# Optimization experiments

Hardware: AMD Instinct MI355X
Metric: run time of the kernel (lower is better)

## Reference

```python
import jax, jax.numpy as jnp
import numpy as np

N_NODES = 100000
N_EDGES = 1600000
NODE_DIM = 128
HIDDEN_DIM = 128


def _sage_conv(x, src, dst, deg_inv, W_l, W_r, b):
    # PyG SAGEConv (aggr='mean', root_weight=True):
    #   out = lin_l(mean_{j in N(i)} x_j) + lin_r(x_i)
    msgs = x[src]                                             # [E, d_in] gather
    agg = jax.ops.segment_sum(msgs, dst, num_segments=N_NODES)  # [N, d_in]
    mean = agg * deg_inv[:, None]
    return mean @ W_l + x @ W_r + b


def setup_inputs() -> dict:
    key = jax.random.key(0)
    ks = jax.random.split(key, 9)
    x = jax.random.normal(ks[0], (N_NODES, NODE_DIM), dtype=jnp.float32)
    edge_index = jax.random.randint(ks[1], (2, N_EDGES), 0, N_NODES, dtype=jnp.int32)
    t = jnp.zeros((1,), dtype=jnp.float32)

    def glorot(k, fan_in, fan_out):
        s = (6.0 / (fan_in + fan_out)) ** 0.5
        return jax.random.uniform(k, (fan_in, fan_out), jnp.float32, -s, s)

    return {
        "t": t,
        "x": x,
        "edge_index": edge_index,
        "W1_l": glorot(ks[2], NODE_DIM, HIDDEN_DIM),
        "W1_r": glorot(ks[3], NODE_DIM, HIDDEN_DIM),
        "b1": jnp.zeros((HIDDEN_DIM,), jnp.float32),
        "W2_l": glorot(ks[4], HIDDEN_DIM, HIDDEN_DIM),
        "W2_r": glorot(ks[5], HIDDEN_DIM, HIDDEN_DIM),
        "b2": jnp.zeros((HIDDEN_DIM,), jnp.float32),
        "W3_l": glorot(ks[6], HIDDEN_DIM, NODE_DIM),
        "W3_r": glorot(ks[7], HIDDEN_DIM, NODE_DIM),
        "b3": jnp.zeros((NODE_DIM,), jnp.float32),
    }


def reference(t, x, edge_index, W1_l, W1_r, b1, W2_l, W2_r, b2, W3_l, W3_r, b3):
    src, dst = edge_index[0], edge_index[1]
    deg = jax.ops.segment_sum(jnp.ones((N_EDGES,), x.dtype), dst, num_segments=N_NODES)
    deg_inv = jnp.where(deg > 0, 1.0 / jnp.maximum(deg, 1.0), 0.0)

    h = jax.nn.relu(_sage_conv(x, src, dst, deg_inv, W1_l, W1_r, b1))
    h = jax.nn.relu(_sage_conv(h, src, dst, deg_inv, W2_l, W2_r, b2))
    dx_dt = _sage_conv(h, src, dst, deg_inv, W3_l, W3_r, b3)
    return dx_dt
```

## Files before the change

kernel.cpp:

```cpp
#include <hip/hip_runtime.h>

#define NN   100000
#define NE   1600000
#define DIM  128
#define NBKT 391
#define EPB  16384
#define NBLK 98
#define NTILES (NN / 16)
#define CASTB 12500
#define CWB   384

typedef short          s16x8 __attribute__((ext_vector_type(8)));
typedef unsigned short u16x8 __attribute__((ext_vector_type(8)));
typedef float          f32x4 __attribute__((ext_vector_type(4)));

__device__ __forceinline__ unsigned short f2b(float f) {
    unsigned u = __float_as_uint(f);
    unsigned r = ((u >> 16) & 1u) + 0x7FFFu;
    return (unsigned short)((u + r) >> 16);
}
__device__ __forceinline__ float b2f(unsigned short h) {
    return __uint_as_float(((unsigned)h) << 16);
}

__global__ void k_prep(const float* __restrict__ x, unsigned short* __restrict__ xb,
                       const int* __restrict__ dst, int* __restrict__ hist,
                       const float* __restrict__ W1l, const float* __restrict__ W1r,
                       const float* __restrict__ W2l, const float* __restrict__ W2r,
                       const float* __restrict__ W3l, const float* __restrict__ W3r,
                       unsigned short* __restrict__ Wt1, unsigned short* __restrict__ Wt2,
                       unsigned short* __restrict__ Wt3) {
    __shared__ int lh[NBKT];
    int t = threadIdx.x, b = blockIdx.x;
    if (b < NBLK) {
        for (int j = t; j < NBKT; j += 256) lh[j] = 0;
        __syncthreads();
        int base = b * EPB;
        int end = base + EPB; if (end > NE) end = NE;
        for (int i = base + t; i < end; i += 256) atomicAdd(&lh[dst[i] >> 8], 1);
        __syncthreads();
        for (int j = t; j < NBKT; j += 256) hist[j * NBLK + b] = lh[j];
    } else if (b < NBLK + CASTB) {
        int i = (b - NBLK) * 256 + t;
        float4 v = ((const float4*)x)[i];
        ushort4 o;
        o.x = f2b(v.x); o.y = f2b(v.y); o.z = f2b(v.z); o.w = f2b(v.w);
        ((ushort4*)xb)[i] = o;
    } else {
        int i = (b - NBLK - CASTB) * 256 + t;
        int L = i >> 15;
        int rem = i & 32767;
        int n = rem >> 8;
        int k = rem & 255;
        const float* Wl = (L == 0) ? W1l : (L == 1) ? W2l : W3l;
        const float* Wr = (L == 0) ? W1r : (L == 1) ? W2r : W3r;
        unsigned short* Wt = (L == 0) ? Wt1 : (L == 1) ? Wt2 : Wt3;
        float v = (k < 128) ? Wl[k * 128 + n] : Wr[(k - 128) * 128 + n];
        Wt[n * 256 + k] = f2b(v);
    }
}

__global__ void k_scanrow(int* __restrict__ hist, int* __restrict__ row_total) {
    __shared__ int sh[128];
    int k = blockIdx.x, t = threadIdx.x;
    int v = (t < NBLK) ? hist[k * NBLK + t] : 0;
    sh[t] = v;
    __syncthreads();
    for (int off = 1; off < 128; off <<= 1) {
        int a = (t >= off) ? sh[t - off] : 0;
        __syncthreads();
        sh[t] += a;
        __syncthreads();
    }
    if (t < NBLK) hist[k * NBLK + t] = sh[t] - v;
    if (t == 127) row_total[k] = sh[127];
}

__global__ void k_scanbkt(const int* __restrict__ row_total, int* __restrict__ bbase) {
    __shared__ int sh[512];
    int t = threadIdx.x;
    int v = (t < NBKT) ? row_total[t] : 0;
    sh[t] = v;
    __syncthreads();
    for (int off = 1; off < 512; off <<= 1) {
        int a = (t >= off) ? sh[t - off] : 0;
        __syncthreads();
        sh[t] += a;
        __syncthreads();
    }
    if (t < NBKT) bbase[t] = sh[t] - v;
    if (t == NBKT) bbase[NBKT] = NE;
}

__global__ void k_bin2(const int* __restrict__ src, const int* __restrict__ dst,
                       const int* __restrict__ hist, const int* __restrict__ bbase,
                       int* __restrict__ binned) {
    __shared__ int s_base[NBKT];
    __shared__ int s_cnt[NBKT];
    int t = threadIdx.x, b = blockIdx.x;
    for (int j = t; j < NBKT; j += 256) {
        s_base[j] = bbase[j] + hist[j * NBLK + b];
        s_cnt[j] = 0;
    }
    __syncthreads();
    int base = b * EPB;
    int end = base + EPB; if (end > NE) end = NE;
    for (int i = base + t; i < end; i += 256) {
        int d = dst[i];
        int k = d >> 8;
        int w = (src[i] << 8) | (d & 255);
        int lpos = atomicAdd(&s_cnt[k], 1);
        binned[s_base[k] + lpos] = w;
    }
}

__global__ void k_build(const int* __restrict__ binned,
                        const int* __restrict__ bucket_base,
                        int* __restrict__ csr,
                        int* __restrict__ row_start, int* __restrict__ deg,
                        float* __restrict__ deg_inv) {
    __shared__ int s_deg[256], s_scan[256], s_cur[256];
    __shared__ int stage[8192];
    int b = blockIdx.x, t = threadIdx.x;
    int base = bucket_base[b], end = bucket_base[b + 1];
    int cnt = end - base;
    s_deg[t] = 0;
    __syncthreads();
    for (int i = t; i < cnt; i += 256)
        atomicAdd(&s_deg[binned[base + i] & 255], 1);
    __syncthreads();
    s_scan[t] = s_deg[t];
    __syncthreads();
    for (int off = 1; off < 256; off <<= 1) {
        int a = (t >= off) ? s_scan[t - off] : 0;
        __syncthreads();
        s_scan[t] += a;
        __syncthreads();
    }
    int excl = s_scan[t] - s_deg[t];
    s_cur[t] = excl;
    int node = b * 256 + t;
    if (node < NN) {
        int d = s_deg[t];
        row_start[node] = base + excl;
        deg[node]       = d;
        deg_inv[node]   = (d > 0) ? 1.0f / (float)d : 0.0f;
    }
    __syncthreads();
    for (int i = t; i < cnt; i += 256) {
        int w = binned[base + i];
        int pos = atomicAdd(&s_cur[w & 255], 1);
        int s = w >> 8;
        if (pos < 8192) stage[pos] = s;
        else            csr[base + pos] = s;
    }
    __syncthreads();
    int m = cnt < 8192 ? cnt : 8192;
    for (int i = t; i < m; i += 256) csr[base + i] = stage[i];
}

__global__ void k_gather(const unsigned short* __restrict__ feat,
                         const int* __restrict__ row_start, const int* __restrict__ deg,
                         const float* __restrict__ deg_inv, const int* __restrict__ csr,
                         unsigned short* __restrict__ mean) {
    int lane = threadIdx.x & 63;
    int wv   = threadIdx.x >> 6;
    int n    = blockIdx.x * 4 + wv;
    int q = lane >> 4, c = lane & 15;
    int base = row_start[n];
    int d    = deg[n];
    float acc0[8], acc1[8];
#pragma unroll
    for (int t = 0; t < 8; t++) { acc0[t] = 0.0f; acc1[t] = 0.0f; }
    const u16x8* fp = (const u16x8*)feat;
    int j = q;
    for (; j + 4 < d; j += 8) {
        int s0 = csr[base + j];
        int s1 = csr[base + j + 4];
        u16x8 v0 = fp[s0 * 16 + c];
        u16x8 v1 = fp[s1 * 16 + c];
#pragma unroll
        for (int t = 0; t < 8; t++) { acc0[t] += b2f(v0[t]); acc1[t] += b2f(v1[t]); }
    }
    if (j < d) {
        int s0 = csr[base + j];
        u16x8 v0 = fp[s0 * 16 + c];
#pragma unroll
        for (int t = 0; t < 8; t++) acc0[t] += b2f(v0[t]);
    }
#pragma unroll
    for (int t = 0; t < 8; t++) acc0[t] += acc1[t];
#pragma unroll
    for (int t = 0; t < 8; t++) {
        acc0[t] += __shfl_xor(acc0[t], 16, 64);
        acc0[t] += __shfl_xor(acc0[t], 32, 64);
    }
    if (q == 0) {
        float s = deg_inv[n];
        u16x8 o;
#pragma unroll
        for (int t = 0; t < 8; t++) o[t] = f2b(acc0[t] * s);
        ((u16x8*)mean)[n * 16 + c] = o;
    }
}

template <int MODE>
__global__ void __launch_bounds__(512)
k_lin(const unsigned short* __restrict__ meanb,
      const unsigned short* __restrict__ hb,
      const unsigned short* __restrict__ Wt,
      const float* __restrict__ bias, void* __restrict__ out) {
    __shared__ s16x8 sW[4096];
    int t = threadIdx.x;
    const s16x8* wp = (const s16x8*)Wt;
#pragma unroll
    for (int it = 0; it < 8; it++) {
        int ci = it * 512 + t;
        int frag = ci >> 6, ln = ci & 63;
        int mt = frag >> 3, kt = frag & 7;
        int m = mt * 16 + (ln & 15);
        int kc = kt * 4 + (ln >> 4);
        sW[ci] = wp[m * 32 + kc];
    }
    __syncthreads();

    int lane = t & 63;
    int wv   = t >> 6;
    int tile = blockIdx.x * 8 + wv;
    if (tile >= NTILES) return;
    int n0 = tile * 16;
    int q = lane >> 4, c = lane & 15;
    const s16x8* mp = (const s16x8*)meanb;
    const s16x8* hp = (const s16x8*)hb;
    int row = n0 + c;
    s16x8 B[8];
#pragma unroll
    for (int kt = 0; kt < 4; kt++) B[kt] = mp[row * 16 + kt * 4 + q];
#pragma unroll
    for (int kt = 0; kt < 4; kt++) B[4 + kt] = hp[row * 16 + kt * 4 + q];
    const f32x4* bp = (const f32x4*)bias;
#pragma unroll
    for (int mt = 0; mt < 8; mt++) {
        f32x4 acc = {0.f, 0.f, 0.f, 0.f};
#pragma unroll
        for (int kt = 0; kt < 8; kt++)
            acc = __builtin_amdgcn_mfma_f32_16x16x32_bf16(sW[(mt * 8 + kt) * 64 + lane],
                                                          B[kt], acc, 0, 0, 0);
        f32x4 bv = bp[mt * 4 + q];
        int node = n0 + c;
        if (MODE == 0) {
            ushort4 o;
            float v0 = acc[0] + bv[0]; if (v0 < 0.f) v0 = 0.f;
            float v1 = acc[1] + bv[1]; if (v1 < 0.f) v1 = 0.f;
            float v2 = acc[2] + bv[2]; if (v2 < 0.f) v2 = 0.f;
            float v3 = acc[3] + bv[3]; if (v3 < 0.f) v3 = 0.f;
            o.x = f2b(v0); o.y = f2b(v1); o.z = f2b(v2); o.w = f2b(v3);
            ((ushort4*)out)[node * 32 + mt * 4 + q] = o;
        } else {
            f32x4 v;
#pragma unroll
            for (int r = 0; r < 4; r++) v[r] = acc[r] + bv[r];
            ((f32x4*)out)[node * 32 + mt * 4 + q] = v;
        }
    }
}

extern "C" void kernel_launch(void* const* d_in, const int* in_sizes, int n_in,
                              void* d_out, int out_size, void* d_ws, size_t ws_size,
                              hipStream_t stream) {
    const float* x   = (const float*)d_in[1];
    const int*   ei  = (const int*)d_in[2];
    const int*   src = ei;
    const int*   dst = ei + NE;
    const float* W1l = (const float*)d_in[3];
    const float* W1r = (const float*)d_in[4];
    const float* b1  = (const float*)d_in[5];
    const float* W2l = (const float*)d_in[6];
    const float* W2r = (const float*)d_in[7];
    const float* b2  = (const float*)d_in[8];
    const float* W3l = (const float*)d_in[9];
    const float* W3r = (const float*)d_in[10];
    const float* b3  = (const float*)d_in[11];

    char* w = (char*)d_ws;
    auto carve = [&](size_t bytes) {
        void* p = (void*)w;
        w += (bytes + 255) & ~(size_t)255;
        return p;
    };
    int*   row_start = (int*)carve(NN * 4);
    int*   deg       = (int*)carve(NN * 4);
    float* deg_inv   = (float*)carve(NN * 4);
    int*   hist      = (int*)carve((size_t)NBKT * NBLK * 4);
    int*   row_total = (int*)carve(NBKT * 4);
    int*   bbase     = (int*)carve((NBKT + 1) * 4);
    int*   csr       = (int*)carve((size_t)NE * 4);
    unsigned short* Wt1 = (unsigned short*)carve(128 * 256 * 2);
    unsigned short* Wt2 = (unsigned short*)carve(128 * 256 * 2);
    unsigned short* Wt3 = (unsigned short*)carve(128 * 256 * 2);
    unsigned short* xb    = (unsigned short*)carve((size_t)NN * DIM * 2);
    unsigned short* meanb = (unsigned short*)carve((size_t)NN * DIM * 2);
    unsigned short* h1b   = (unsigned short*)carve((size_t)NN * DIM * 2);
    unsigned short* h2b   = xb;
    int*   binned    = (int*)meanb;

    k_prep<<<NBLK + CASTB + CWB, 256, 0, stream>>>(x, xb, dst, hist,
                                                   W1l, W1r, W2l, W2r, W3l, W3r,
                                                   Wt1, Wt2, Wt3);
    k_scanrow<<<NBKT, 128, 0, stream>>>(hist, row_total);
    k_scanbkt<<<1, 512, 0, stream>>>(row_total, bbase);
    k_bin2<<<NBLK, 256, 0, stream>>>(src, dst, hist, bbase, binned);
    k_build<<<NBKT, 256, 0, stream>>>(binned, bbase, csr, row_start, deg, deg_inv);

    const int GB = NN / 4;
    const int LB = (NTILES + 7) / 8;

    k_gather<<<GB, 256, 0, stream>>>(xb, row_start, deg, deg_inv, csr, meanb);
    k_lin<0><<<LB, 512, 0, stream>>>(meanb, xb, Wt1, b1, (void*)h1b);
    k_gather<<<GB, 256, 0, stream>>>(h1b, row_start, deg, deg_inv, csr, meanb);
    k_lin<0><<<LB, 512, 0, stream>>>(meanb, h1b, Wt2, b2, (void*)h2b);
    k_gather<<<GB, 256, 0, stream>>>(h2b, row_start, deg, deg_inv, csr, meanb);
    k_lin<1><<<LB, 512, 0, stream>>>(meanb, h2b, Wt3, b3, d_out);
}
```

Measured before the change: 451.6 us.

## Fuse CSR preprocessing kernels into one cooperative kernel with grid syncs

Replaces the five preprocessing launches (histogram/cast, row scan, bucket scan, binning, CSR build) with a single cooperative kernel of 512 blocks that separates the phases with grid-wide syncs. Edges are repartitioned across 512 blocks instead of 98, so the histogram and binning phases use more of the GPU, and the row scan now handles 512 entries per bucket. This removes per-launch overhead and idle gaps between the small kernels. In exchange, each grid sync has a cost, the cast loops become grid-stride, and correctness depends on all 512 blocks being co-resident.

```diff
diff --git a/kernel.cpp b/kernel.cpp
--- a/kernel.cpp
+++ b/kernel.cpp
@@ -1,14 +1,17 @@
 #include <hip/hip_runtime.h>
+#include <hip/hip_cooperative_groups.h>
+
+namespace cg = cooperative_groups;
 
 #define NN   100000
 #define NE   1600000
 #define DIM  128
 #define NBKT 391
-#define EPB  16384
-#define NBLK 98
+#define GRID 512
+#define EPB3 (NE / GRID)
+#define NX4  (NN * DIM / 4)
+#define NWELE (3 * 128 * 256)
 #define NTILES (NN / 16)
-#define CASTB 12500
-#define CWB   384
 
 typedef short          s16x8 __attribute__((ext_vector_type(8)));
 typedef unsigned short u16x8 __attribute__((ext_vector_type(8)));
@@ -23,140 +26,140 @@
     return __uint_as_float(((unsigned)h) << 16);
 }
 
-__global__ void k_prep(const float* __restrict__ x, unsigned short* __restrict__ xb,
-                       const int* __restrict__ dst, int* __restrict__ hist,
-                       const float* __restrict__ W1l, const float* __restrict__ W1r,
-                       const float* __restrict__ W2l, const float* __restrict__ W2r,
-                       const float* __restrict__ W3l, const float* __restrict__ W3r,
-                       unsigned short* __restrict__ Wt1, unsigned short* __restrict__ Wt2,
-                       unsigned short* __restrict__ Wt3) {
-    __shared__ int lh[NBKT];
+__global__ void __launch_bounds__(256)
+k_prep_all(const float* __restrict__ x, unsigned short* __restrict__ xb,
+           const int* __restrict__ src, const int* __restrict__ dst,
+           int* __restrict__ hist, int* __restrict__ row_total,
+           int* __restrict__ bbase, int* __restrict__ binned, int* __restrict__ csr,
+           int* __restrict__ row_start, int* __restrict__ deg,
+           float* __restrict__ deg_inv,
+           const float* __restrict__ W1l, const float* __restrict__ W1r,
+           const float* __restrict__ W2l, const float* __restrict__ W2r,
+           const float* __restrict__ W3l, const float* __restrict__ W3r,
+           unsigned short* __restrict__ Wt1, unsigned short* __restrict__ Wt2,
+           unsigned short* __restrict__ Wt3) {
+    __shared__ int shm[8960];
+    cg::grid_group grid = cg::this_grid();
     int t = threadIdx.x, b = blockIdx.x;
-    if (b < NBLK) {
+    int e0 = b * EPB3, e1 = e0 + EPB3;
+
+    {
+        int* lh = shm;
         for (int j = t; j < NBKT; j += 256) lh[j] = 0;
         __syncthreads();
-        int base = b * EPB;
-        int end = base + EPB; if (end > NE) end = NE;
-        for (int i = base + t; i < end; i += 256) atomicAdd(&lh[dst[i] >> 8], 1);
-        __syncthreads();
-        for (int j = t; j < NBKT; j += 256) hist[j * NBLK + b] = lh[j];
-    } else if (b < NBLK + CASTB) {
-        int i = (b - NBLK) * 256 + t;
-        float4 v = ((const float4*)x)[i];
-        ushort4 o;
-        o.x = f2b(v.x); o.y = f2b(v.y); o.z = f2b(v.z); o.w = f2b(v.w);
-        ((ushort4*)xb)[i] = o;
-    } else {
-        int i = (b - NBLK - CASTB) * 256 + t;
-        int L = i >> 15;
-        int rem = i & 32767;
-        int n = rem >> 8;
-        int k = rem & 255;
-        const float* Wl = (L == 0) ? W1l : (L == 1) ? W2l : W3l;
-        const float* Wr = (L == 0) ? W1r : (L == 1) ? W2r : W3r;
-        unsigned short* Wt = (L == 0) ? Wt1 : (L == 1) ? Wt2 : Wt3;
-        float v = (k < 128) ? Wl[k * 128 + n] : Wr[(k - 128) * 128 + n];
-        Wt[n * 256 + k] = f2b(v);
-    }
-}
-
-__global__ void k_scanrow(int* __restrict__ hist, int* __restrict__ row_total) {
-    __shared__ int sh[128];
-    int k = blockIdx.x, t = threadIdx.x;
-    int v = (t < NBLK) ? hist[k * NBLK + t] : 0;
-    sh[t] = v;
-    __syncthreads();
-    for (int off = 1; off < 128; off <<= 1) {
-        int a = (t >= off) ? sh[t - off] : 0;
-        __syncthreads();
-        sh[t] += a;
-        __syncthreads();
-    }
-    if (t < NBLK) hist[k * NBLK + t] = sh[t] - v;
-    if (t == 127) row_total[k] = sh[127];
-}
-
-__global__ void k_scanbkt(const int* __restrict__ row_total, int* __restrict__ bbase) {
-    __shared__ int sh[512];
-    int t = threadIdx.x;
-    int v = (t < NBKT) ? row_total[t] : 0;
-    sh[t] = v;
-    __syncthreads();
-    for (int off = 1; off < 512; off <<= 1) {
-        int a = (t >= off) ? sh[t - off] : 0;
-        __syncthreads();
-        sh[t] += a;
-        __syncthreads();
-    }
-    if (t < NBKT) bbase[t] = sh[t] - v;
-    if (t == NBKT) bbase[NBKT] = NE;
-}
-
-__global__ void k_bin2(const int* __restrict__ src, const int* __restrict__ dst,
-                       const int* __restrict__ hist, const int* __restrict__ bbase,
-                       int* __restrict__ binned) {
-    __shared__ int s_base[NBKT];
-    __shared__ int s_cnt[NBKT];
-    int t = threadIdx.x, b = blockIdx.x;
-    for (int j = t; j < NBKT; j += 256) {
-        s_base[j] = bbase[j] + hist[j * NBLK + b];
-        s_cnt[j] = 0;
-    }
-    __syncthreads();
-    int base = b * EPB;
-    int end = base + EPB; if (end > NE) end = NE;
-    for (int i = base + t; i < end; i += 256) {
-        int d = dst[i];
-        int k = d >> 8;
-        int w = (src[i] << 8) | (d & 255);
-        int lpos = atomicAdd(&s_cnt[k], 1);
-        binned[s_base[k] + lpos] = w;
-    }
-}
-
-__global__ void k_build(const int* __restrict__ binned,
-                        const int* __restrict__ bucket_base,
-                        int* __restrict__ csr,
-                        int* __restrict__ row_start, int* __restrict__ deg,
-                        float* __restrict__ deg_inv) {
-    __shared__ int s_deg[256], s_scan[256], s_cur[256];
-    __shared__ int stage[8192];
-    int b = blockIdx.x, t = threadIdx.x;
-    int base = bucket_base[b], end = bucket_base[b + 1];
-    int cnt = end - base;
-    s_deg[t] = 0;
-    __syncthreads();
-    for (int i = t; i < cnt; i += 256)
-        atomicAdd(&s_deg[binned[base + i] & 255], 1);
-    __syncthreads();
-    s_scan[t] = s_deg[t];
-    __syncthreads();
-    for (int off = 1; off < 256; off <<= 1) {
-        int a = (t >= off) ? s_scan[t - off] : 0;
-        __syncthreads();
-        s_scan[t] += a;
-        __syncthreads();
-    }
-    int excl = s_scan[t] - s_deg[t];
-    s_cur[t] = excl;
-    int node = b * 256 + t;
-    if (node < NN) {
-        int d = s_deg[t];
-        row_start[node] = base + excl;
-        deg[node]       = d;
-        deg_inv[node]   = (d > 0) ? 1.0f / (float)d : 0.0f;
-    }
-    __syncthreads();
-    for (int i = t; i < cnt; i += 256) {
-        int w = binned[base + i];
-        int pos = atomicAdd(&s_cur[w & 255], 1);
-        int s = w >> 8;
-        if (pos < 8192) stage[pos] = s;
-        else            csr[base + pos] = s;
-    }
-    __syncthreads();
-    int m = cnt < 8192 ? cnt : 8192;
-    for (int i = t; i < m; i += 256) csr[base + i] = stage[i];
+        for (int i = e0 + t; i < e1; i += 256) atomicAdd(&lh[dst[i] >> 8], 1);
+        for (int i = b * 256 + t; i < NX4; i += GRID * 256) {
+            float4 v = ((const float4*)x)[i];
+            ushort4 o;
+            o.x = f2b(v.x); o.y = f2b(v.y); o.z = f2b(v.z); o.w = f2b(v.w);
+            ((ushort4*)xb)[i] = o;
+        }
+        for (int i = b * 256 + t; i < NWELE; i += GRID * 256) {
+            int L = i >> 15, rem = i & 32767, n = rem >> 8, k = rem & 255;
+            const float* Wl = (L == 0) ? W1l : (L == 1) ? W2l : W3l;
+            const float* Wr = (L == 0) ? W1r : (L == 1) ? W2r : W3r;
+            unsigned short* Wt = (L == 0) ? Wt1 : (L == 1) ? Wt2 : Wt3;
+            float v = (k < 128) ? Wl[k * 128 + n] : Wr[(k - 128) * 128 + n];
+            Wt[n * 256 + k] = f2b(v);
+        }
+        __syncthreads();
+        for (int j = t; j < NBKT; j += 256) hist[j * GRID + b] = lh[j];
+    }
+    grid.sync();
+
+    if (b < NBKT) {
+        int* P0 = shm; int* P1 = shm + 256;
+        int i0 = b * GRID + t * 2;
+        int v0 = hist[i0], v1 = hist[i0 + 1];
+        int s = v0 + v1;
+        P0[t] = s;
+        int* cur = P0; int* nxt = P1;
+        for (int off = 1; off < 256; off <<= 1) {
+            __syncthreads();
+            nxt[t] = cur[t] + (t >= off ? cur[t - off] : 0);
+            int* tmp = cur; cur = nxt; nxt = tmp;
+        }
+        __syncthreads();
+        int incl = cur[t];
+        int excl = incl - s;
+        hist[i0]     = excl;
+        hist[i0 + 1] = excl + v0;
+        if (t == 255) row_total[b] = incl;
+    }
+    grid.sync();
+
+    if (b == 0) {
+        int* A0 = shm; int* A1 = shm + 512;
+        for (int i = t; i < 512; i += 256) A0[i] = (i < NBKT) ? row_total[i] : 0;
+        int* cur = A0; int* nxt = A1;
+        for (int off = 1; off < 512; off <<= 1) {
+            __syncthreads();
+            for (int i = t; i < 512; i += 256)
+                nxt[i] = cur[i] + (i >= off ? cur[i - off] : 0);
+            int* tmp = cur; cur = nxt; nxt = tmp;
+        }
+        __syncthreads();
+        for (int i = t; i < NBKT; i += 256) bbase[i] = (i == 0) ? 0 : cur[i - 1];
+        if (t == 0) bbase[NBKT] = NE;
+    }
+    grid.sync();
+
+    {
+        int* s_base = shm; int* s_cnt = shm + NBKT;
+        for (int j = t; j < NBKT; j += 256) {
+            s_base[j] = bbase[j] + hist[j * GRID + b];
+            s_cnt[j] = 0;
+        }
+        __syncthreads();
+        for (int i = e0 + t; i < e1; i += 256) {
+            int d = dst[i];
+            int k = d >> 8;
+            int w = (src[i] << 8) | (d & 255);
+            int lpos = atomicAdd(&s_cnt[k], 1);
+            binned[s_base[k] + lpos] = w;
+        }
+    }
+    grid.sync();
+
+    if (b < NBKT) {
+        int* s_deg = shm; int* s_scan = shm + 256; int* s_cur = shm + 512;
+        int* stage = shm + 768;
+        int base = bbase[b], end = bbase[b + 1];
+        int cnt = end - base;
+        s_deg[t] = 0;
+        __syncthreads();
+        for (int i = t; i < cnt; i += 256)
+            atomicAdd(&s_deg[binned[base + i] & 255], 1);
+        __syncthreads();
+        s_scan[t] = s_deg[t];
+        __syncthreads();
+        for (int off = 1; off < 256; off <<= 1) {
+            int a = (t >= off) ? s_scan[t - off] : 0;
+            __syncthreads();
+            s_scan[t] += a;
+            __syncthreads();
+        }
+        int excl = s_scan[t] - s_deg[t];
+        s_cur[t] = excl;
+        int node = b * 256 + t;
+        if (node < NN) {
+            int d = s_deg[t];
+            row_start[node] = base + excl;
+            deg[node]       = d;
+            deg_inv[node]   = (d > 0) ? 1.0f / (float)d : 0.0f;
+        }
+        __syncthreads();
+        for (int i = t; i < cnt; i += 256) {
+            int w = binned[base + i];
+            int pos = atomicAdd(&s_cur[w & 255], 1);
+            int s = w >> 8;
+            if (pos < 8192) stage[pos] = s;
+            else            csr[base + pos] = s;
+        }
+        __syncthreads();
+        int m = cnt < 8192 ? cnt : 8192;
+        for (int i = t; i < m; i += 256) csr[base + i] = stage[i];
+    }
 }
 
 __global__ void k_gather(const unsigned short* __restrict__ feat,
@@ -291,7 +294,7 @@
     int*   row_start = (int*)carve(NN * 4);
     int*   deg       = (int*)carve(NN * 4);
     float* deg_inv   = (float*)carve(NN * 4);
-    int*   hist      = (int*)carve((size_t)NBKT * NBLK * 4);
+    int*   hist      = (int*)carve((size_t)NBKT * GRID * 4);
     int*   row_total = (int*)carve(NBKT * 4);
     int*   bbase     = (int*)carve((NBKT + 1) * 4);
     int*   csr       = (int*)carve((size_t)NE * 4);
@@ -304,13 +307,15 @@
     unsigned short* h2b   = xb;
     int*   binned    = (int*)meanb;
 
-    k_prep<<<NBLK + CASTB + CWB, 256, 0, stream>>>(x, xb, dst, hist,
-                                                   W1l, W1r, W2l, W2r, W3l, W3r,
-                                                   Wt1, Wt2, Wt3);
-    k_scanrow<<<NBKT, 128, 0, stream>>>(hist, row_total);
-    k_scanbkt<<<1, 512, 0, stream>>>(row_total, bbase);
-    k_bin2<<<NBLK, 256, 0, stream>>>(src, dst, hist, bbase, binned);
-    k_build<<<NBKT, 256, 0, stream>>>(binned, bbase, csr, row_start, deg, deg_inv);
+    void* args[] = {
+        (void*)&x, (void*)&xb, (void*)&src, (void*)&dst,
+        (void*)&hist, (void*)&row_total, (void*)&bbase, (void*)&binned, (void*)&csr,
+        (void*)&row_start, (void*)&deg, (void*)&deg_inv,
+        (void*)&W1l, (void*)&W1r, (void*)&W2l, (void*)&W2r, (void*)&W3l, (void*)&W3r,
+        (void*)&Wt1, (void*)&Wt2, (void*)&Wt3
+    };
+    hipLaunchCooperativeKernel((const void*)k_prep_all, dim3(GRID), dim3(256),
+                               args, 0, stream);
 
     const int GB = NN / 4;
     const int LB = (NTILES + 7) / 8;
```

Result: slower. 702.3 us (+55.5%).
